# Kernel optimization log

Measured on AMD Instinct MI355X. Metric: run time of the kernel, lower is better.

Reference implementation:

```python
import jax, jax.numpy as jnp
import numpy as np

HEADS = 8
HD = 64            # hidden_channels per head
WIN = 16 * 16      # prod(window_size)
SCALE = HD ** -0.5


def setup_inputs() -> dict:
    key = jax.random.key(0)
    ks = jax.random.split(key, 8)
    B, C, H, W = 2, 128, 128, 128
    ROT = 32
    x = jax.random.normal(ks[0], (B, C, H, W), jnp.float32)
    skip = jax.random.normal(ks[1], (B, C, H, W), jnp.float32)
    ang = jax.random.uniform(ks[2], (H, W, ROT), jnp.float32) * 6.2831853
    sin = jnp.sin(ang)
    cos = jnp.cos(ang)
    Wq = jax.random.normal(ks[3], (HEADS * HD, C), jnp.float32) * 0.05
    Wkv = jax.random.normal(ks[4], (2 * HEADS * HD, C), jnp.float32) * 0.05
    Wout = jax.random.normal(ks[5], (C, HEADS * HD), jnp.float32) * 0.05
    return {"x": x, "skip": skip, "sin": sin, "cos": cos,
            "Wq": Wq, "Wkv": Wkv, "Wout": Wout}


def _rotate_half_pairs(t):
    # torch: reshape(..., -1, 2); stack([-even, odd], -1); reshape back
    t2 = t.reshape(t.shape[:-1] + (-1, 2))
    return jnp.stack([-t2[..., 0], t2[..., 1]], axis=-1).reshape(t.shape)


def reference(x, skip, sin, cos, Wq, Wkv, Wout):
    B, C, H, W = x.shape
    rot = sin.shape[-1]

    # 1x1 convs (no bias) as channel contractions
    q = jnp.einsum('oc,bchw->bohw', Wq, x)                 # [B, heads*hd, H, W]
    kv_input = jnp.concatenate([x, skip], axis=0)          # [2B, C, H, W]
    kv = jnp.einsum('oc,bchw->bohw', Wkv, kv_input)        # [2B, 2*heads*hd, H, W]
    k, v = jnp.split(kv, 2, axis=1)

    # faithful raw reshape (memory reinterpretation, as in the source)
    def rs(t):
        return t.reshape(HEADS * t.shape[0], H, W, -1)
    q, k, v = rs(q), rs(k), rs(v)

    # inline RoPE (faithful, including the `k = k + cos` quirk of the source)
    q_r, q_pass = q[..., :rot], q[..., rot:]
    k_r, k_pass = k[..., :rot], k[..., rot:]
    q_r = q_r * cos + _rotate_half_pairs(q_r) * sin
    k_r = k_r + cos + _rotate_half_pairs(k_r) * sin
    q = jnp.concatenate([q_r, q_pass], axis=-1)
    k = jnp.concatenate([k_r, k_pass], axis=-1)

    def towin(t):
        n = int(np.prod(t.shape[:-1])) // WIN
        return t.reshape(n, WIN, t.shape[-1])
    q, k, v = towin(q), towin(k), towin(v)

    # skip-KV concat: halve window-batch, double window length
    k = k.reshape(k.shape[0] // 2, 2 * WIN, k.shape[2])
    v = v.reshape(v.shape[0] // 2, 2 * WIN, v.shape[2])

    sim = jnp.einsum('bid,bjd->bij', q, k) * SCALE
    attn = jax.nn.softmax(sim, axis=-1)
    out = jnp.einsum('bij,bjd->bid', attn, v)

    out = out.reshape(B, HEADS * out.shape[2], H, W)       # faithful raw reshape
    out = jnp.einsum('oc,bchw->bohw', Wout, out)           # [B, C, H, W]
    return out
```

## Files before the change

kernel.cpp:

```cpp
#include <hip/hip_runtime.h>
#include <hip/hip_bf16.h>


typedef unsigned short u16;
using bfrag = __attribute__((ext_vector_type(8))) short;
using ffrag = __attribute__((ext_vector_type(4))) float;
using s4v   = __attribute__((ext_vector_type(4))) short;
using u32x4 = __attribute__((ext_vector_type(4))) unsigned int;

#define MFMA16(a, b, c) __builtin_amdgcn_mfma_f32_16x16x32_bf16((a), (b), (c), 0, 0, 0)

__device__ __forceinline__ u16 f2bf(float f) {
    __hip_bfloat16 h = __float2bfloat16(f);
    u16 u;
    __builtin_memcpy(&u, &h, 2);
    return u;
}

__device__ __forceinline__ int sw(int p) { return (p ^ (p >> 3)) & 15; }

__global__ __launch_bounds__(256) void k_prep(
    const float* __restrict__ Wq, const float* __restrict__ Wkv,
    const float* __restrict__ Wout, u16* __restrict__ WB, u16* __restrict__ WoutB)
{
    int i8 = (blockIdx.x * 256 + threadIdx.x) * 8;
    const float* src;
    u16* dst;
    if (i8 < 65536)       { src = Wq + i8;            dst = WB + i8; }
    else if (i8 < 196608) { src = Wkv + (i8 - 65536); dst = WB + i8; }
    else                  { src = Wout + (i8 - 196608); dst = WoutB + (i8 - 196608); }
    float4 a = *(const float4*)src;
    float4 b = *(const float4*)(src + 4);
    u16 tmp[8];
    tmp[0] = f2bf(a.x); tmp[1] = f2bf(a.y); tmp[2] = f2bf(a.z); tmp[3] = f2bf(a.w);
    tmp[4] = f2bf(b.x); tmp[5] = f2bf(b.y); tmp[6] = f2bf(b.z); tmp[7] = f2bf(b.w);
    *(uint4*)dst = *(uint4*)tmp;
}

__global__ __launch_bounds__(256) void k_cast(
    const float* __restrict__ x, const float* __restrict__ skip,
    u16* __restrict__ xb)
{
    __shared__ float LT[128 * 65];
    const int t = threadIdx.x;
    const int pos0 = blockIdx.x * 64;
    const int p = blockIdx.y;
    const float* src = (p < 2) ? (x + (size_t)p * 2097152)
                               : (skip + (size_t)(p - 2) * 2097152);
    u16* dst = xb + (size_t)p * 2097152;

#pragma unroll
    for (int it = 0; it < 8; ++it) {
        int idx = it * 256 + t;
        int c = idx >> 4, p4 = (idx & 15) * 4;
        float4 v = *(const float4*)(src + (size_t)c * 16384 + pos0 + p4);
        LT[c * 65 + p4 + 0] = v.x;
        LT[c * 65 + p4 + 1] = v.y;
        LT[c * 65 + p4 + 2] = v.z;
        LT[c * 65 + p4 + 3] = v.w;
    }
    __syncthreads();

#pragma unroll
    for (int it = 0; it < 4; ++it) {
        int g = it * 256 + t;
        int pos_l = g >> 4, chunk = g & 15;
        u16 tmp[8];
#pragma unroll
        for (int j = 0; j < 8; ++j)
            tmp[j] = f2bf(LT[(chunk * 8 + j) * 65 + pos_l]);
        *(uint4*)(dst + (size_t)(pos0 + pos_l) * 128 + chunk * 8) = *(uint4*)tmp;
    }
}

__global__ __launch_bounds__(256, 4) void k_proj(
    const u16* __restrict__ xb, const float* __restrict__ sinp,
    const float* __restrict__ cosp, const u16* __restrict__ WB,
    u16* __restrict__ qb, u16* __restrict__ kbuf, u16* __restrict__ vbuf)
{
    __shared__ u16 BT[64 * 128];
    __shared__ float2 SC2[64][33];
    const int t = threadIdx.x;
    const int pos0 = blockIdx.x * 64;
    const int tr = blockIdx.y;
    const int w = t >> 6, l = t & 63, lr = l & 15, lg = l >> 4;

    int WBrow, plane, mode;
    u16* dst;
    const bool contig = (tr >= 8);
    if (tr < 8) {
        int b = tr >> 2, o0 = (tr & 3) * 128;
        WBrow = o0; plane = b; mode = 1;
        dst = qb + (size_t)b * 8388608 + (size_t)o0 * 16384;
    } else {
        int t2 = tr - 8;
        int bkv = t2 >> 3, oo0 = (t2 & 7) * 128;
        WBrow = 512 + oo0; plane = bkv;
        if (oo0 < 512) {
            dst = kbuf + (size_t)bkv * 8388608 + (size_t)blockIdx.x * 32768 + (size_t)oo0 * 64;
            mode = 2;
        } else {
            dst = vbuf + (size_t)bkv * 8388608 + (size_t)blockIdx.x * 32768 + (size_t)(oo0 - 512) * 64;
            mode = 0;
        }
    }

    const u16* xsrc = xb + (size_t)plane * 2097152 + (size_t)pos0 * 128;
#pragma unroll
    for (int it = 0; it < 4; ++it) {
        int li = it * 256 + t;
        int row = li >> 4, chunk = li & 15;
        uint4 v = *(const uint4*)(xsrc + (size_t)row * 128 + chunk * 8);
        *(uint4*)&BT[row * 128 + ((chunk ^ sw(row)) << 3)] = v;
    }

    const int hh = pos0 >> 7;
    const int wwhi = blockIdx.x & 1;
    if (mode != 0) {
        const int hb = hh >> 6;
        const int ridx = (hh & 63) * 2 + wwhi;
#pragma unroll
        for (int e = 0; e < 2; ++e) {
            int g = e * 256 + t;
            int row = g >> 3;
            int q = g & 7;
            size_t base = ((size_t)(row * 2 + hb) * 128 + ridx) * 32 + q * 4;
            float4 sv4 = *(const float4*)(sinp + base);
            float4 cv4 = *(const float4*)(cosp + base);
            SC2[row][q * 4 + 0] = float2{sv4.x, cv4.x};
            SC2[row][q * 4 + 1] = float2{sv4.y, cv4.y};
            SC2[row][q * 4 + 2] = float2{sv4.z, cv4.z};
            SC2[row][q * 4 + 3] = float2{sv4.w, cv4.w};
        }
    }

    ffrag zf = {0.f, 0.f, 0.f, 0.f};
    ffrag acc[4][2];
#pragma unroll
    for (int mb = 0; mb < 4; ++mb)
#pragma unroll
        for (int nb = 0; nb < 2; ++nb) acc[mb][nb] = zf;

    __syncthreads();

#pragma unroll
    for (int kk = 0; kk < 4; ++kk) {
        bfrag A[4], B[2];
#pragma unroll
        for (int mb = 0; mb < 4; ++mb) {
            int pos_l = mb * 16 + lr;
            A[mb] = *(const bfrag*)&BT[pos_l * 128 + (((kk * 4 + lg) ^ sw(pos_l)) << 3)];
        }
#pragma unroll
        for (int nb = 0; nb < 2; ++nb)
            B[nb] = *(const bfrag*)(WB + (size_t)(WBrow + w * 32 + nb * 16 + lr) * 128 + kk * 32 + lg * 8);
#pragma unroll
        for (int mb = 0; mb < 4; ++mb)
#pragma unroll
            for (int nb = 0; nb < 2; ++nb)
                acc[mb][nb] = MFMA16(A[mb], B[nb], acc[mb][nb]);
    }

    __syncthreads();

#pragma unroll
    for (int mb = 0; mb < 4; ++mb) {
        const bool roped = (mode != 0) && (mb < 2);
#pragma unroll
        for (int nb = 0; nb < 2; ++nb) {
            int o_l = w * 32 + nb * 16 + lr;
            int p0 = mb * 16 + lg * 4;
            ffrag v4 = acc[mb][nb];
            if (roped) {
                const int ob63 = o_l & 63;
#pragma unroll
                for (int r = 0; r < 4; ++r) {
                    float2 sc = SC2[ob63][p0 + r];
                    float sg = (r & 1) ? sc.x : -sc.x;
                    v4[r] = (mode == 1) ? v4[r] * (sc.y + sg)
                                        : v4[r] * (1.f + sg) + sc.y;
                }
            }
            s4v pk;
            pk[0] = (short)f2bf(v4[0]); pk[1] = (short)f2bf(v4[1]);
            pk[2] = (short)f2bf(v4[2]); pk[3] = (short)f2bf(v4[3]);
            int slot = p0 >> 3;
            *(s4v*)&BT[o_l * 64 + ((slot ^ (o_l & 7)) << 3) + (p0 & 4)] = pk;
        }
    }

#pragma unroll
    for (int it = 0; it < 4; ++it) {
        int i = it * 64 + l;
        int row = w * 32 + (i >> 3);
        int slot = i & 7;
        u32x4 v = *(const u32x4*)&BT[row * 64 + ((slot ^ (row & 7)) << 3)];
        size_t goff = contig ? ((size_t)row * 64 + slot * 8)
                             : ((size_t)row * 16384 + pos0 + slot * 8);
        __builtin_nontemporal_store(v, (u32x4*)(dst + goff));
    }
}

__global__ __launch_bounds__(256) void k_attn(
    const u16* __restrict__ qb, const u16* __restrict__ kbuf,
    const u16* __restrict__ vbuf, u16* __restrict__ ob)
{
    __shared__ u16 Ks[64 * 64];
    __shared__ u16 Vt[64 * 64];
    __shared__ u16 Ps[4][64 * 40];
    __shared__ float Lbuf[256];

    const int bp = blockIdx.x;
    const int t = threadIdx.x, w = t >> 6, l = t & 63, lr = l & 15, lg = l >> 4;

    const u16* Qg = qb + (size_t)bp * 16384 + w * 4096;

    bfrag Qf[4][2];
#pragma unroll
    for (int rb = 0; rb < 4; ++rb)
#pragma unroll
        for (int dk = 0; dk < 2; ++dk)
            Qf[rb][dk] = *(const bfrag*)(Qg + (rb * 16 + lr) * 64 + dk * 32 + lg * 8);

    ffrag zf = {0.f, 0.f, 0.f, 0.f};
    ffrag Oacc[4][4];
#pragma unroll
    for (int rb = 0; rb < 4; ++rb)
#pragma unroll
        for (int sb = 0; sb < 4; ++sb) Oacc[rb][sb] = zf;
    float Lp[4] = {0.f, 0.f, 0.f, 0.f};

    const int srow = t >> 2, sq = t & 3;
    const size_t kvoff = (size_t)(bp >> 8) * 8388608 + (size_t)(bp & 255) * 128;
    const u16* gK = kbuf + kvoff;
    const u16* gV = vbuf + kvoff;
    #define KVOFF(c) ((size_t)(((c) & 3) * 64 + srow) * 32768 + (size_t)(((c) >> 2) * 64) + sq * 16)

    uint4 k0 = *(const uint4*)(gK + KVOFF(0));
    uint4 k1 = *(const uint4*)(gK + KVOFF(0) + 8);
    uint4 v0 = *(const uint4*)(gV + KVOFF(0));
    uint4 v1 = *(const uint4*)(gV + KVOFF(0) + 8);

    const int chv = srow >> 3, jl = srow & 7;

    for (int c = 0; c < 8; ++c) {
        __syncthreads();
        *(uint4*)&Ks[srow * 64 + (((sq * 2) ^ (srow & 7)) << 3)] = k0;
        *(uint4*)&Ks[srow * 64 + (((sq * 2 + 1) ^ (srow & 7)) << 3)] = k1;
        {
            u16 tmp[16];
            *(uint4*)&tmp[0] = v0;
            *(uint4*)&tmp[8] = v1;
#pragma unroll
            for (int e = 0; e < 16; ++e) {
                int d = sq * 16 + e;
                int s = (d & 7) ^ ((d >> 3) & 7);
                Vt[d * 64 + ((chv ^ s) << 3) + jl] = tmp[e];
            }
        }
        __syncthreads();
        if (c < 7) {
            k0 = *(const uint4*)(gK + KVOFF(c + 1));
            k1 = *(const uint4*)(gK + KVOFF(c + 1) + 8);
            v0 = *(const uint4*)(gV + KVOFF(c + 1));
            v1 = *(const uint4*)(gV + KVOFF(c + 1) + 8);
        }

#pragma unroll
        for (int jh = 0; jh < 2; ++jh) {
#pragma unroll
            for (int jtl = 0; jtl < 2; ++jtl) {
                const int jt = jh * 2 + jtl;
                bfrag Kf[2];
#pragma unroll
                for (int dk = 0; dk < 2; ++dk)
                    Kf[dk] = *(const bfrag*)&Ks[(jt * 16 + lr) * 64 + (((dk * 4 + lg) ^ (lr & 7)) << 3)];
#pragma unroll
                for (int rb = 0; rb < 4; ++rb) {
                    ffrag sf = zf;
                    __builtin_amdgcn_s_setprio(1);
                    sf = MFMA16(Kf[0], Qf[rb][0], sf);
                    sf = MFMA16(Kf[1], Qf[rb][1], sf);
                    __builtin_amdgcn_s_setprio(0);
                    float e0 = __expf(sf[0] * 0.125f);
                    float e1 = __expf(sf[1] * 0.125f);
                    float e2 = __expf(sf[2] * 0.125f);
                    float e3 = __expf(sf[3] * 0.125f);
                    Lp[rb] += (e0 + e1) + (e2 + e3);
                    s4v pk;
                    pk[0] = (short)f2bf(e0); pk[1] = (short)f2bf(e1);
                    pk[2] = (short)f2bf(e2); pk[3] = (short)f2bf(e3);
                    *(s4v*)&Ps[w][(rb * 16 + lr) * 40 + jtl * 16 + lg * 4] = pk;
                }
            }

            bfrag Vf[4];
#pragma unroll
            for (int sb = 0; sb < 4; ++sb) {
                int d = sb * 16 + lr;
                int s = (d & 7) ^ ((d >> 3) & 7);
                Vf[sb] = *(const bfrag*)&Vt[d * 64 + (((jh * 4 + lg) ^ s) << 3)];
            }
            __builtin_amdgcn_s_setprio(1);
#pragma unroll
            for (int rb = 0; rb < 4; ++rb) {
                bfrag Pf = *(const bfrag*)&Ps[w][(rb * 16 + lr) * 40 + lg * 8];
#pragma unroll
                for (int sb = 0; sb < 4; ++sb)
                    Oacc[rb][sb] = MFMA16(Pf, Vf[sb], Oacc[rb][sb]);
            }
            __builtin_amdgcn_s_setprio(0);
        }
    }
    #undef KVOFF

#pragma unroll
    for (int rb = 0; rb < 4; ++rb) {
        float v = Lp[rb];
        v += __shfl_xor(v, 16);
        v += __shfl_xor(v, 32);
        if (lg == 0) Lbuf[w * 64 + rb * 16 + lr] = v;
    }
    u16* og = ob + (size_t)bp * 16384 + w * 4096;
#pragma unroll
    for (int rb = 0; rb < 4; ++rb)
#pragma unroll
        for (int r = 0; r < 4; ++r) {
            float inv = 1.f / Lbuf[w * 64 + rb * 16 + lg * 4 + r];
#pragma unroll
            for (int sb = 0; sb < 4; ++sb)
                og[(rb * 16 + lg * 4 + r) * 64 + sb * 16 + lr] = f2bf(Oacc[rb][sb][r] * inv);
        }
}

__global__ __launch_bounds__(256) void k_out(
    const u16* __restrict__ ob, const u16* __restrict__ WoutB,
    float* __restrict__ out)
{
    __shared__ u16 OT[64 * 128];
    const int t = threadIdx.x, w = t >> 6, l = t & 63, lr = l & 15, lg = l >> 4;
    const int pos0 = blockIdx.x * 64;
    const int b = blockIdx.y;
    const u16* obp = ob + (size_t)b * 8388608;
    float* op = out + (size_t)b * 2097152;

    ffrag zf = {0.f, 0.f, 0.f, 0.f};
    ffrag acc[2][4];
#pragma unroll
    for (int rb = 0; rb < 2; ++rb)
#pragma unroll
        for (int nb = 0; nb < 4; ++nb) acc[rb][nb] = zf;

    for (int kc = 0; kc < 4; ++kc) {
        __syncthreads();
#pragma unroll
        for (int it = 0; it < 4; ++it) {
            int g = it * 256 + t;
            int cl = g >> 3, pk = g & 7;
            uint4 v = *(const uint4*)(obp + (size_t)(kc * 128 + cl) * 16384 + pos0 + pk * 8);
            u16 tmp[8];
            *(uint4*)tmp = v;
#pragma unroll
            for (int e = 0; e < 8; ++e) {
                int pos_l = pk * 8 + e;
                OT[pos_l * 128 + (((cl >> 3) ^ sw(pos_l)) << 3) + (cl & 7)] = tmp[e];
            }
        }
        __syncthreads();

#pragma unroll
        for (int kk = 0; kk < 4; ++kk) {
            bfrag Af[2];
#pragma unroll
            for (int rb = 0; rb < 2; ++rb)
                Af[rb] = *(const bfrag*)(WoutB + (size_t)(w * 32 + rb * 16 + lr) * 512 + kc * 128 + kk * 32 + lg * 8);
#pragma unroll
            for (int nb = 0; nb < 4; ++nb) {
                int pos_l = nb * 16 + lr;
                bfrag B = *(const bfrag*)&OT[pos_l * 128 + (((kk * 4 + lg) ^ sw(pos_l)) << 3)];
#pragma unroll
                for (int rb = 0; rb < 2; ++rb)
                    acc[rb][nb] = MFMA16(Af[rb], B, acc[rb][nb]);
            }
        }
    }

#pragma unroll
    for (int rb = 0; rb < 2; ++rb)
#pragma unroll
        for (int nb = 0; nb < 4; ++nb)
#pragma unroll
            for (int r = 0; r < 4; ++r)
                __builtin_nontemporal_store(acc[rb][nb][r],
                    op + (size_t)(w * 32 + rb * 16 + lg * 4 + r) * 16384 + pos0 + nb * 16 + lr);
}

extern "C" void kernel_launch(void* const* d_in, const int* in_sizes, int n_in,
                              void* d_out, int out_size, void* d_ws, size_t ws_size,
                              hipStream_t stream) {
    const float* x    = (const float*)d_in[0];
    const float* skip = (const float*)d_in[1];
    const float* sinp = (const float*)d_in[2];
    const float* cosp = (const float*)d_in[3];
    const float* Wq   = (const float*)d_in[4];
    const float* Wkv  = (const float*)d_in[5];
    const float* Wout = (const float*)d_in[6];
    float* out = (float*)d_out;

    u16* qb    = (u16*)d_ws;
    u16* kbp   = qb + (size_t)16777216;
    u16* vbp   = kbp + (size_t)33554432;
    u16* xbp   = vbp + (size_t)33554432;
    u16* WBp   = xbp + (size_t)8388608;
    u16* WoutB = WBp + (size_t)196608;

    hipLaunchKernelGGL(k_prep, dim3(128), dim3(256), 0, stream,
                       Wq, Wkv, Wout, WBp, WoutB);
    hipLaunchKernelGGL(k_cast, dim3(256, 4), dim3(256), 0, stream,
                       x, skip, xbp);
    hipLaunchKernelGGL(k_proj, dim3(256, 40), dim3(256), 0, stream,
                       xbp, sinp, cosp, WBp, qb, kbp, vbp);
    hipLaunchKernelGGL(k_attn, dim3(1024), dim3(256), 0, stream,
                       qb, kbp, vbp, qb );
    hipLaunchKernelGGL(k_out, dim3(256, 2), dim3(256), 0, stream,
                       qb, WoutB, out);
}
```

Baseline: 151.5 us.

## Fuse fp32-to-bf16 input cast into projection kernel and fold softmax scale into Q

The separate k_cast kernel is removed; k_proj now reads fp32 x/skip directly, transposes through a shared buffer (reused for sin/cos) and converts to bf16 itself. This drops one launch and the bf16 intermediate round trip, but each of the 40 y-blocks per position tile now redoes the fp32 load and transpose (each input plane is re-read by many blocks), and shared memory use grows, which may lower occupancy. Separately, Q is pre-multiplied by scale*log2(e) so attention can use exp2f instead of scaling before __expf.

```diff
diff --git a/kernel.cpp b/kernel.cpp
--- a/kernel.cpp
+++ b/kernel.cpp
@@ -9,6 +9,7 @@
 using u32x4 = __attribute__((ext_vector_type(4))) unsigned int;
 
 #define MFMA16(a, b, c) __builtin_amdgcn_mfma_f32_16x16x32_bf16((a), (b), (c), 0, 0, 0)
+#define QSCALE 0.1803368801111204f
 
 __device__ __forceinline__ u16 f2bf(float f) {
     __hip_bfloat16 h = __float2bfloat16(f);
@@ -37,49 +38,16 @@
     *(uint4*)dst = *(uint4*)tmp;
 }
 
-__global__ __launch_bounds__(256) void k_cast(
+__global__ __launch_bounds__(256, 4) void k_proj(
     const float* __restrict__ x, const float* __restrict__ skip,
-    u16* __restrict__ xb)
-{
-    __shared__ float LT[128 * 65];
-    const int t = threadIdx.x;
-    const int pos0 = blockIdx.x * 64;
-    const int p = blockIdx.y;
-    const float* src = (p < 2) ? (x + (size_t)p * 2097152)
-                               : (skip + (size_t)(p - 2) * 2097152);
-    u16* dst = xb + (size_t)p * 2097152;
-
-#pragma unroll
-    for (int it = 0; it < 8; ++it) {
-        int idx = it * 256 + t;
-        int c = idx >> 4, p4 = (idx & 15) * 4;
-        float4 v = *(const float4*)(src + (size_t)c * 16384 + pos0 + p4);
-        LT[c * 65 + p4 + 0] = v.x;
-        LT[c * 65 + p4 + 1] = v.y;
-        LT[c * 65 + p4 + 2] = v.z;
-        LT[c * 65 + p4 + 3] = v.w;
-    }
-    __syncthreads();
-
-#pragma unroll
-    for (int it = 0; it < 4; ++it) {
-        int g = it * 256 + t;
-        int pos_l = g >> 4, chunk = g & 15;
-        u16 tmp[8];
-#pragma unroll
-        for (int j = 0; j < 8; ++j)
-            tmp[j] = f2bf(LT[(chunk * 8 + j) * 65 + pos_l]);
-        *(uint4*)(dst + (size_t)(pos0 + pos_l) * 128 + chunk * 8) = *(uint4*)tmp;
-    }
-}
-
-__global__ __launch_bounds__(256, 4) void k_proj(
-    const u16* __restrict__ xb, const float* __restrict__ sinp,
-    const float* __restrict__ cosp, const u16* __restrict__ WB,
+    const float* __restrict__ sinp, const float* __restrict__ cosp,
+    const u16* __restrict__ WB,
     u16* __restrict__ qb, u16* __restrict__ kbuf, u16* __restrict__ vbuf)
 {
     __shared__ u16 BT[64 * 128];
-    __shared__ float2 SC2[64][33];
+    __shared__ __align__(16) float UN[128 * 65];
+    float2 (*SC2)[33] = (float2(*)[33])UN;
+
     const int t = threadIdx.x;
     const int pos0 = blockIdx.x * 64;
     const int tr = blockIdx.y;
@@ -105,14 +73,31 @@
         }
     }
 
-    const u16* xsrc = xb + (size_t)plane * 2097152 + (size_t)pos0 * 128;
+    const float* src = (plane < 2) ? (x + (size_t)plane * 2097152)
+                                   : (skip + (size_t)(plane - 2) * 2097152);
+#pragma unroll
+    for (int it = 0; it < 8; ++it) {
+        int idx = it * 256 + t;
+        int c = idx >> 4, p4 = (idx & 15) * 4;
+        float4 v = *(const float4*)(src + (size_t)c * 16384 + pos0 + p4);
+        UN[c * 65 + p4 + 0] = v.x;
+        UN[c * 65 + p4 + 1] = v.y;
+        UN[c * 65 + p4 + 2] = v.z;
+        UN[c * 65 + p4 + 3] = v.w;
+    }
+    __syncthreads();
+
 #pragma unroll
     for (int it = 0; it < 4; ++it) {
-        int li = it * 256 + t;
-        int row = li >> 4, chunk = li & 15;
-        uint4 v = *(const uint4*)(xsrc + (size_t)row * 128 + chunk * 8);
-        *(uint4*)&BT[row * 128 + ((chunk ^ sw(row)) << 3)] = v;
-    }
+        int g = it * 256 + t;
+        int pos_l = g >> 4, chunk = g & 15;
+        u16 tmp[8];
+#pragma unroll
+        for (int j = 0; j < 8; ++j)
+            tmp[j] = f2bf(UN[(chunk * 8 + j) * 65 + pos_l]);
+        *(uint4*)&BT[pos_l * 128 + ((chunk ^ sw(pos_l)) << 3)] = *(uint4*)tmp;
+    }
+    __syncthreads();
 
     const int hh = pos0 >> 7;
     const int wwhi = blockIdx.x & 1;
@@ -141,8 +126,6 @@
 #pragma unroll
         for (int nb = 0; nb < 2; ++nb) acc[mb][nb] = zf;
 
-    __syncthreads();
-
 #pragma unroll
     for (int kk = 0; kk < 4; ++kk) {
         bfrag A[4], B[2];
@@ -180,6 +163,10 @@
                     v4[r] = (mode == 1) ? v4[r] * (sc.y + sg)
                                         : v4[r] * (1.f + sg) + sc.y;
                 }
+            }
+            if (mode == 1) {
+#pragma unroll
+                for (int r = 0; r < 4; ++r) v4[r] *= QSCALE;
             }
             s4v pk;
             pk[0] = (short)f2bf(v4[0]); pk[1] = (short)f2bf(v4[1]);
@@ -282,10 +269,10 @@
                     sf = MFMA16(Kf[0], Qf[rb][0], sf);
                     sf = MFMA16(Kf[1], Qf[rb][1], sf);
                     __builtin_amdgcn_s_setprio(0);
-                    float e0 = __expf(sf[0] * 0.125f);
-                    float e1 = __expf(sf[1] * 0.125f);
-                    float e2 = __expf(sf[2] * 0.125f);
-                    float e3 = __expf(sf[3] * 0.125f);
+                    float e0 = exp2f(sf[0]);
+                    float e1 = exp2f(sf[1]);
+                    float e2 = exp2f(sf[2]);
+                    float e3 = exp2f(sf[3]);
                     Lp[rb] += (e0 + e1) + (e2 + e3);
                     s4v pk;
                     pk[0] = (short)f2bf(e0); pk[1] = (short)f2bf(e1);
@@ -410,16 +397,13 @@
     u16* qb    = (u16*)d_ws;
     u16* kbp   = qb + (size_t)16777216;
     u16* vbp   = kbp + (size_t)33554432;
-    u16* xbp   = vbp + (size_t)33554432;
-    u16* WBp   = xbp + (size_t)8388608;
+    u16* WBp   = vbp + (size_t)33554432;
     u16* WoutB = WBp + (size_t)196608;
 
     hipLaunchKernelGGL(k_prep, dim3(128), dim3(256), 0, stream,
                        Wq, Wkv, Wout, WBp, WoutB);
-    hipLaunchKernelGGL(k_cast, dim3(256, 4), dim3(256), 0, stream,
-                       x, skip, xbp);
     hipLaunchKernelGGL(k_proj, dim3(256, 40), dim3(256), 0, stream,
-                       xbp, sinp, cosp, WBp, qb, kbp, vbp);
+                       x, skip, sinp, cosp, WBp, qb, kbp, vbp);
     hipLaunchKernelGGL(k_attn, dim3(1024), dim3(256), 0, stream,
                        qb, kbp, vbp, qb );
     hipLaunchKernelGGL(k_out, dim3(256, 2), dim3(256), 0, stream,
```

Measured after the change: 163.9 us. 8.2% more time.
